# Kernel tuning notes

Measured on AMD Instinct MI355X. Metric: run time of the kernel, lower is better.

## Reference

```python
import jax, jax.numpy as jnp
import numpy as np

DEPTH = 4
EPS = 1e-05


def _hard_sigmoid(x):
    # Keras hard_sigmoid: clip(0.2*x + 0.5, 0, 1)
    return jnp.clip(0.2 * x + 0.5, 0.0, 1.0)


def _ln(x, gamma, beta):
    m = jnp.mean(x, axis=-1, keepdims=True)
    std = jnp.sqrt(jnp.var(x, axis=-1, keepdims=True) + EPS)
    return gamma * ((x - m) / (std + EPS)) + beta


def setup_inputs() -> dict:
    key = jax.random.key(0)
    ks = jax.random.split(key, 4)
    B, T, Din, H = 64, 256, 512, 512
    D = Din + H
    O = 2 * H + Din
    x = jax.random.normal(ks[0], (B, T, Din), dtype=jnp.float32)
    mask = jnp.ones((B, T), dtype=bool)
    W = jax.random.normal(ks[1], (D, O), dtype=jnp.float32) * (1.0 / np.sqrt(D))
    U = jax.random.normal(ks[2], (D, O), dtype=jnp.float32) * (1.0 / np.sqrt(D))
    b = jnp.zeros((O,), dtype=jnp.float32)
    gammas = jnp.ones((2, O), dtype=jnp.float32)
    betas = jnp.zeros((2, O), dtype=jnp.float32)
    return {"x": x, "mask": mask, "W": W, "U": U, "b": b,
            "gammas": gammas, "betas": betas, "bucket_size": 256}


def _forward(x, mask, W, U, b, gammas, betas, bucket_size):
    B, T, Din = x.shape
    D = W.shape[0]            # Din + H
    H = W.shape[1] - D        # hidden_dim
    # pad x with zeros in the hidden slots: (B,T,D) -> time-major (Tb,B,D)
    xp = jnp.concatenate([x, jnp.zeros((B, T, H), x.dtype)], axis=-1)
    xs = jnp.transpose(xp, (1, 0, 2))[:bucket_size]           # (Tb,B,D)
    m = jnp.transpose(mask, (1, 0))[:bucket_size]             # (Tb,B) bool
    # mask2 = mask * (1 - shift_left(mask)) : marks the last valid position
    m_shift = jnp.concatenate([m[1:], jnp.zeros((1, B), bool)], axis=0)
    m2 = jnp.logical_and(m, jnp.logical_not(m_shift))          # (Tb,B)
    mf = m.astype(x.dtype)[:, :, None]                         # (Tb,B,1)
    m2f = m2[:, :, None]                                       # (Tb,B,1) bool

    g0, g1 = gammas[0], gammas[1]
    be0, be1 = betas[0], betas[1]

    def hstep(carry, inp):
        h_tm1, fk_tm1 = carry
        xt, fkp, mt, m2t = inp
        sum1 = _ln(xt @ W, g0, be0)
        sum2 = _ln(h_tm1 @ U, g1, be1)
        total = sum1 + sum2 + b
        fk_c = _hard_sigmoid(total[:, :D])                     # (B,D)
        h_ = jnp.tanh(total[:, D:])                            # (B,H)
        h_pad = jnp.concatenate([jnp.zeros((xt.shape[0], D - H), xt.dtype), h_], axis=-1)
        h_cand = (1.0 - fk_c) * xt + fk_c * h_pad
        h = fkp * h_tm1 + (1.0 - fkp) * h_cand
        fk = fkp + (1.0 - fkp) * fk_c
        fk = jnp.where(m2t, 0.0, fk)
        out_h = mt * h + (1.0 - mt) * h_tm1
        out_fk = mt * fk + (1.0 - mt) * fk_tm1
        return (out_h, out_fk), (out_h, out_fk)

    Tb = xs.shape[0]
    fk_prev = jnp.zeros((Tb, B, D), x.dtype)
    h_seq = xs
    for _ in range(DEPTH):
        init = (jnp.zeros((B, D), x.dtype), jnp.zeros((B, D), x.dtype))
        _, (h_seq, fk_seq) = jax.lax.scan(hstep, init, (h_seq, fk_prev, mf, m2f))
        fk_prev = jnp.concatenate([fk_seq[1:], jnp.zeros((1, B, D), x.dtype)], axis=0)
    # outputs = last depth, last timestep, hidden slice
    return h_seq[-1, :, Din:]                                  # (B,H)


def reference(x, mask, W, U, b, gammas, betas, bucket_size):
    return _forward(x, mask, W, U, b, gammas, betas, bucket_size)
```

## Files before the change

### kernel.cpp

```cpp
#include <hip/hip_runtime.h>
#include <hip/hip_bf16.h>
#include <math.h>

#define B_   64
#define T_   256
#define DIN_ 512
#define H_   512
#define D_   1024
#define O_   1536
#define TB_  (T_*B_)
#define EPSf 1e-5f
#define NWG  96
#define NSLOT (T_ + 6)

typedef short  bf16x8 __attribute__((ext_vector_type(8)));
typedef float  f32x4  __attribute__((ext_vector_type(4)));
typedef ushort u16x4  __attribute__((ext_vector_type(4)));
typedef unsigned long long ull;

#define SPLIT1(f, Hm, Lm) { __hip_bfloat16 _h = __float2bfloat16(f); (Hm) = *(ushort*)&_h; \
    __hip_bfloat16 _l = __float2bfloat16((f) - __bfloat162float(_h)); (Lm) = *(ushort*)&_l; }

__device__ inline void st_f32_coh(float* p, float v) {
    __hip_atomic_store(p, v, __ATOMIC_RELAXED, __HIP_MEMORY_SCOPE_AGENT);
}
__device__ inline void st_u16_coh(ushort* p, ushort v) {
    __hip_atomic_store(p, v, __ATOMIC_RELAXED, __HIP_MEMORY_SCOPE_AGENT);
}
__device__ inline void st_u32_coh(unsigned* p, unsigned v) {
    __hip_atomic_store(p, v, __ATOMIC_RELAXED, __HIP_MEMORY_SCOPE_AGENT);
}
__device__ inline void st_f32x2_coh(float* p, float a, float b) {
    union { float f[2]; ull u; } pk;
    pk.f[0] = a; pk.f[1] = b;
    __hip_atomic_store((ull*)p, pk.u, __ATOMIC_RELAXED, __HIP_MEMORY_SCOPE_AGENT);
}

__global__ __launch_bounds__(256) void k_mask(const int* __restrict__ mask,
                                              int* __restrict__ mcode) {
    int g = blockIdx.x * 256 + threadIdx.x;
    int t = g >> 6, b = g & 63;
    int mt = mask[b * T_ + t] != 0;
    int mn = (t + 1 < T_) ? (mask[b * T_ + t + 1] != 0) : 0;
    mcode[g] = mt | (mn << 1);
}

__global__ __launch_bounds__(256) void k_prepx(const float* __restrict__ x,
                                               ushort* __restrict__ Xh) {
    int g  = blockIdx.x * 256 + threadIdx.x;
    int i4 = g * 4;
    int row = i4 >> 10;
    int k   = i4 & 1023;
    int t = row >> 6, b = row & 63;
    float4 v = make_float4(0.f, 0.f, 0.f, 0.f);
    if (k < 512) v = *(const float4*)&x[((size_t)b * T_ + t) * 512 + k];
    u16x4 h;
    __hip_bfloat16 b0 = __float2bfloat16(v.x); h[0] = *(ushort*)&b0;
    __hip_bfloat16 b1 = __float2bfloat16(v.y); h[1] = *(ushort*)&b1;
    __hip_bfloat16 b2 = __float2bfloat16(v.z); h[2] = *(ushort*)&b2;
    __hip_bfloat16 b3 = __float2bfloat16(v.w); h[3] = *(ushort*)&b3;
    *(u16x4*)&Xh[i4] = h;
}

__global__ __launch_bounds__(256) void k_prep(const float* __restrict__ M,
                                              ushort* __restrict__ Mt_hi,
                                              ushort* __restrict__ Mt_lo) {
    __shared__ float ls[64][65];
    int k0 = blockIdx.y * 64;
    int o0 = blockIdx.x * 64;
    int tid = threadIdx.x;
    int r = tid >> 2, cq = tid & 3;
#pragma unroll
    for (int j = 0; j < 4; ++j) {
        float4 v = *(const float4*)&M[(size_t)(k0 + r) * O_ + o0 + cq * 16 + j * 4];
        ls[r][cq * 16 + j * 4 + 0] = v.x;
        ls[r][cq * 16 + j * 4 + 1] = v.y;
        ls[r][cq * 16 + j * 4 + 2] = v.z;
        ls[r][cq * 16 + j * 4 + 3] = v.w;
    }
    __syncthreads();
    int ol = tid >> 2, kq = tid & 3;
    ushort th[16], tl[16];
#pragma unroll
    for (int j = 0; j < 16; ++j) {
        float v = ls[kq * 16 + j][ol];
        SPLIT1(v, th[j], tl[j]);
    }
    size_t base = (size_t)(o0 + ol) * D_ + k0 + kq * 16;
    *(int4*)&Mt_hi[base]     = *(int4*)&th[0];
    *(int4*)&Mt_hi[base + 8] = *(int4*)&th[8];
    *(int4*)&Mt_lo[base]     = *(int4*)&tl[0];
    *(int4*)&Mt_lo[base + 8] = *(int4*)&tl[8];
}

__device__ inline void gbar(unsigned* __restrict__ fl, int w, unsigned bar) {
    __syncthreads();
    asm volatile("s_waitcnt vmcnt(0)" ::: "memory");
    if (threadIdx.x == 0)
        __hip_atomic_store(&fl[w], bar, __ATOMIC_RELAXED, __HIP_MEMORY_SCOPE_AGENT);
    if (threadIdx.x < NWG) {
        while (__hip_atomic_load(&fl[threadIdx.x], __ATOMIC_RELAXED,
                                 __HIP_MEMORY_SCOPE_AGENT) < bar)
            __builtin_amdgcn_s_sleep(2);
    }
    __syncthreads();
    __builtin_amdgcn_fence(__ATOMIC_ACQUIRE, "agent");
}

__global__ __launch_bounds__(256, 1) void k_pipe(
        const float* __restrict__ x,
        const ushort* __restrict__ Xbh,
        ushort* __restrict__ Xrh,
        ushort* __restrict__ Hbh,
        float* __restrict__ Y1, float* __restrict__ Y2,
        float* __restrict__ pstats, float* __restrict__ finals,
        unsigned* __restrict__ ftag, unsigned* __restrict__ flags,
        const ushort* __restrict__ Uth, const ushort* __restrict__ Utl,
        const ushort* __restrict__ Wth, const ushort* __restrict__ Wtl,
        const float* __restrict__ gam, const float* __restrict__ bet,
        const float* __restrict__ bias,
        const int* __restrict__ mcode, float* __restrict__ out) {
    __shared__ __hip_bfloat16 lds[4 * 16 * 1024];
    __shared__ f32x4 ldsc[2][64][2];
    const int bx = blockIdx.x;
    const int dom = bx / NWG;
    const int w   = bx % NWG;
    const int tid = threadIdx.x;
    const int lane = tid & 63;
    const int wv = tid >> 6;
    const int rt = wv & 1;
    const int kh = wv >> 1;
    const int lr = lane & 15;
    const int lg = lane >> 4;
    const int c0 = w * 16;
    const int br0 = dom * 32 + rt * 16;
    unsigned* fl = flags + dom * 128;
    float* pst   = pstats + (size_t)dom * 4 * 32 * NWG * 4;
    float* fin   = finals + (size_t)dom * 128 * 4;
    unsigned* ft = ftag + (size_t)dom * 128;

    {
        int cl = tid >> 4, kc = tid & 15;
        const ushort* srcs0 = Uth + (size_t)(c0 + cl) * D_ + kc * 64;
        const ushort* srcs1 = Utl + (size_t)(c0 + cl) * D_ + kc * 64;
        const ushort* srcs2 = Wth + (size_t)(c0 + cl) * D_ + kc * 64;
        const ushort* srcs3 = Wtl + (size_t)(c0 + cl) * D_ + kc * 64;
        char* base = (char*)lds;
#pragma unroll
        for (int j = 0; j < 8; ++j) {
            int k = kc * 64 + j * 8;
            int off = (cl * 2048 + k * 2) ^ ((cl & 7) << 4);
            *(int4*)(base + off)           = *(const int4*)(srcs0 + j * 8);
            *(int4*)(base + 32768 + off)   = *(const int4*)(srcs1 + j * 8);
            *(int4*)(base + 65536 + off)   = *(const int4*)(srcs2 + j * 8);
            *(int4*)(base + 98304 + off)   = *(const int4*)(srcs3 + j * 8);
        }
    }
    __syncthreads();

    const int d = c0 + lr;
    const bool gate_w = (w < 64);
    const bool tanh_w = (w >= 32 && w < 64);
    float g0d = 0.f, g1d = 0.f, cd = 0.f, g0e = 0.f, g1e = 0.f, ce = 0.f;
    if (gate_w) {
        g0d = gam[d]; g1d = gam[O_ + d];
        cd  = bet[d] + bet[O_ + d] + bias[d];
    }
    if (tanh_w) {
        int e = d + 512;
        g0e = gam[e]; g1e = gam[O_ + e];
        ce  = bet[e] + bet[O_ + e] + bias[e];
    }

    float h1r[4][4] = {}, fk1r[4][4] = {};
    float oh_d1[4][4] = {}, oh_d2[4][4] = {}, fkp_d1[4][4] = {};
    f32x4 acc1[4], acc2[4];

    unsigned bar = 0;
    for (int s = 0; s < NSLOT; ++s) {
#pragma unroll
        for (int l = 0; l < 4; ++l) {
            int t = s - 2 * l;
            bool act = (t >= 0) && (t < T_);
            f32x4 p1 = {0,0,0,0}, p2 = {0,0,0,0};
            if (act) {
                const ushort* xsh;
                if (l == 0) {
                    xsh = Xbh + ((size_t)t * B_ + br0 + lr) * D_ + kh * 512;
                } else {
                    xsh = Xrh + (((size_t)l * 3 + (t % 3)) * B_ + br0 + lr) * D_ + kh * 512;
                }
                const ushort* hsh = Hbh + ((size_t)l * B_ + br0 + lr) * D_ + kh * 512;
                const char* lb = (const char*)lds;
                f32x4 a10 = {0,0,0,0}, a11 = {0,0,0,0};
                f32x4 a20 = {0,0,0,0}, a21 = {0,0,0,0};
#pragma unroll 4
                for (int kc = 0; kc < 16; ++kc) {
                    int kloc = kc * 32 + lg * 8;
                    int kglob = kh * 512 + kloc;
                    int off = (lr * 2048 + kglob * 2) ^ ((lr & 7) << 4);
                    bf16x8 xa = *(const bf16x8*)(xsh + kloc);
                    bf16x8 ha = *(const bf16x8*)(hsh + kloc);
                    bf16x8 ubh = *(const bf16x8*)(lb + off);
                    bf16x8 ubl = *(const bf16x8*)(lb + 32768 + off);
                    bf16x8 wbh = *(const bf16x8*)(lb + 65536 + off);
                    bf16x8 wbl = *(const bf16x8*)(lb + 98304 + off);
                    a10 = __builtin_amdgcn_mfma_f32_16x16x32_bf16(xa, wbh, a10, 0, 0, 0);
                    a11 = __builtin_amdgcn_mfma_f32_16x16x32_bf16(xa, wbl, a11, 0, 0, 0);
                    a20 = __builtin_amdgcn_mfma_f32_16x16x32_bf16(ha, ubh, a20, 0, 0, 0);
                    a21 = __builtin_amdgcn_mfma_f32_16x16x32_bf16(ha, ubl, a21, 0, 0, 0);
                }
                p1 = a10 + a11;
                p2 = a20 + a21;
                if (kh == 1) { ldsc[rt][lane][0] = p1; ldsc[rt][lane][1] = p2; }
            }
            __syncthreads();
            if (act && kh == 0) {
                f32x4 o1 = ldsc[rt][lane][0], o2 = ldsc[rt][lane][1];
                acc1[l] = p1 + o1;
                acc2[l] = p2 + o2;
#pragma unroll
                for (int j = 0; j < 4; ++j) {
                    float s1 = acc1[l][j], q1 = s1 * s1;
                    float s2 = acc2[l][j], q2 = s2 * s2;
#pragma unroll
                    for (int m = 1; m < 16; m <<= 1) {
                        s1 += __shfl_xor(s1, m); q1 += __shfl_xor(q1, m);
                        s2 += __shfl_xor(s2, m); q2 += __shfl_xor(q2, m);
                    }
                    if (lr == 0) {
                        int lrow = rt * 16 + lg * 4 + j;
                        float* sp = &pst[(((size_t)l * 32 + lrow) * NWG + w) * 4];
                        st_f32x2_coh(sp, s1, q1);
                        st_f32x2_coh(sp + 2, s2, q2);
                    }
                }
                if (w >= 64) {
                    int cexp = c0 + lr - 1024;
#pragma unroll
                    for (int j = 0; j < 4; ++j) {
                        int b = br0 + lg * 4 + j;
                        st_f32_coh(&Y1[((size_t)l * B_ + b) * 512 + cexp], acc1[l][j]);
                        st_f32_coh(&Y2[((size_t)l * B_ + b) * 512 + cexp], acc2[l][j]);
                    }
                }
            }
            __syncthreads();
        }
        gbar(fl, w, ++bar);

        if (wv < 2) {
            int pair = w + NWG * wv;
            if (pair < 128) {
                const float* pp = &pst[(size_t)pair * NWG * 4];
                float s1 = 0.f, q1 = 0.f, s2 = 0.f, q2 = 0.f;
                if (lane < 32) {
#pragma unroll
                    for (int i = 0; i < 3; ++i) {
                        float4 v = *(const float4*)(pp + (lane + i * 32) * 4);
                        s1 += v.x; q1 += v.y; s2 += v.z; q2 += v.w;
                    }
                }
#pragma unroll
                for (int m = 1; m < 32; m <<= 1) {
                    s1 += __shfl_xor(s1, m); q1 += __shfl_xor(q1, m);
                    s2 += __shfl_xor(s2, m); q2 += __shfl_xor(q2, m);
                }
                if (lane == 0) {
                    float m1 = s1 * (1.f / O_);
                    float v1 = q1 * (1.f / O_) - m1 * m1;
                    float i1 = 1.f / (sqrtf(v1 + EPSf) + EPSf);
                    float m2 = s2 * (1.f / O_);
                    float v2 = q2 * (1.f / O_) - m2 * m2;
                    float i2 = 1.f / (sqrtf(v2 + EPSf) + EPSf);
                    st_f32x2_coh(&fin[(size_t)pair * 4], m1, i1);
                    st_f32x2_coh(&fin[(size_t)pair * 4 + 2], m2, i2);
                    asm volatile("s_waitcnt vmcnt(0)" ::: "memory");
                    st_u32_coh(&ft[pair], (unsigned)(s + 1));
                }
            }
        }

        if (gate_w && wv < 2) {
#pragma unroll
            for (int li = 0; li < 4; ++li) {
                const int l = 3 - li;
                const int lp = (l > 0) ? l - 1 : 0;
                int t = s - 2 * l;
                bool act = (t >= 0) && (t < T_);
                float ohn[4], ofkn[4];
                if (act) {
                    int b_base = dom * 32 + wv * 16 + lg * 4;
                    int4 mc4 = *(const int4*)&mcode[t * B_ + b_base];
                    int mcarr[4] = {mc4.x, mc4.y, mc4.z, mc4.w};
#pragma unroll
                    for (int j = 0; j < 4; ++j) {
                        int b = b_base + j;
                        int lrow = wv * 16 + lg * 4 + j;
                        int pair = l * 32 + lrow;
                        while (__hip_atomic_load(&ft[pair], __ATOMIC_RELAXED,
                                                 __HIP_MEMORY_SCOPE_AGENT) < (unsigned)(s + 1))
                            __builtin_amdgcn_s_sleep(1);
                        union { ull u[2]; float f[4]; } fv;
                        fv.u[0] = __hip_atomic_load((ull*)&fin[(size_t)pair * 4],
                                                    __ATOMIC_RELAXED, __HIP_MEMORY_SCOPE_AGENT);
                        fv.u[1] = __hip_atomic_load((ull*)&fin[(size_t)pair * 4 + 2],
                                                    __ATOMIC_RELAXED, __HIP_MEMORY_SCOPE_AGENT);
                        float m1 = fv.f[0], i1 = fv.f[1], m2 = fv.f[2], i2 = fv.f[3];
                        float y1 = acc1[l][j], y2 = acc2[l][j];
                        float td = g0d * (y1 - m1) * i1 + g1d * (y2 - m2) * i2 + cd;
                        float fkc = fminf(fmaxf(0.2f * td + 0.5f, 0.f), 1.f);
                        float hpad = 0.f;
                        if (tanh_w) {
                            float y1e = Y1[((size_t)l * B_ + b) * 512 + (d - 512)];
                            float y2e = Y2[((size_t)l * B_ + b) * 512 + (d - 512)];
                            float te = g0e * (y1e - m1) * i1 + g1e * (y2e - m2) * i2 + ce;
                            hpad = tanhf(te);
                        }
                        float xt;
                        if (l == 0)
                            xt = (d < 512) ? x[((size_t)b * T_ + t) * 512 + d] : 0.f;
                        else
                            xt = oh_d2[lp][j];
                        float fkp = (l > 0 && t + 1 < T_) ? fkp_d1[lp][j] : 0.f;
                        float hc = (1.f - fkc) * xt + fkc * hpad;
                        float h  = fkp * h1r[l][j] + (1.f - fkp) * hc;
                        float fk = fkp + (1.f - fkp) * fkc;
                        int mt = mcarr[j] & 1, mn = (mcarr[j] >> 1) & 1;
                        if (mt && !mn) fk = 0.f;
                        float oh  = mt ? h  : h1r[l][j];
                        float ofk = mt ? fk : fk1r[l][j];
                        h1r[l][j] = oh; fk1r[l][j] = ofk;
                        __hip_bfloat16 hb = __float2bfloat16(oh);
                        ushort hi = *(ushort*)&hb;
                        st_u16_coh(Hbh + ((size_t)l * B_ + b) * D_ + d, hi);
                        if (l < 3) {
                            size_t xb = (((size_t)(l + 1) * 3 + (t % 3)) * B_ + b) * D_ + d;
                            st_u16_coh(Xrh + xb, hi);
                        }
                        if (l == 3 && t == T_ - 1 && d >= 512)
                            out[(size_t)b * 512 + (d - 512)] = oh;
                        ohn[j] = oh; ofkn[j] = ofk;
                    }
                }
#pragma unroll
                for (int j = 0; j < 4; ++j) {
                    oh_d2[l][j] = oh_d1[l][j];
                    if (act) { oh_d1[l][j] = ohn[j]; fkp_d1[l][j] = ofkn[j]; }
                }
            }
        }
        gbar(fl, w, ++bar);
    }
}

extern "C" void kernel_launch(void* const* d_in, const int* in_sizes, int n_in,
                              void* d_out, int out_size, void* d_ws, size_t ws_size,
                              hipStream_t stream) {
    (void)in_sizes; (void)n_in; (void)out_size;
    const float* x      = (const float*)d_in[0];
    const int*   mask   = (const int*)d_in[1];
    const float* W      = (const float*)d_in[2];
    const float* U      = (const float*)d_in[3];
    const float* bias   = (const float*)d_in[4];
    const float* gammas = (const float*)d_in[5];
    const float* betas  = (const float*)d_in[6];

    float* ws = (float*)d_ws;
    float* Y1    = ws;
    float* Y2    = Y1 + (size_t)4 * B_ * 512;
    float* pstats = Y2 + (size_t)4 * B_ * 512;
    float* finals = pstats + (size_t)2 * 4 * 32 * NWG * 4;
    unsigned* ftag  = (unsigned*)(finals + 2 * 128 * 4);
    unsigned* flags = ftag + 2 * 128;
    int* mcode = (int*)(flags + 256);
    ushort* Xbh = (ushort*)(mcode + TB_);
    ushort* Xrh = Xbh + (size_t)TB_ * D_;
    ushort* Hbh = Xrh + (size_t)4 * 3 * B_ * D_;
    ushort* Uth = Hbh + (size_t)4 * B_ * D_;
    ushort* Utl = Uth + (size_t)O_ * D_;
    ushort* Wth = Utl + (size_t)O_ * D_;
    ushort* Wtl = Wth + (size_t)O_ * D_;
    size_t need_bytes = ((char*)(Wtl + (size_t)O_ * D_)) - ((char*)d_ws);
    if (ws_size < need_bytes) return;

    k_prepx<<<TB_ * D_ / 4 / 256, 256, 0, stream>>>(x, Xbh);
    k_mask<<<TB_ / 256, 256, 0, stream>>>(mask, mcode);
    k_prep<<<dim3(O_ / 64, D_ / 64), 256, 0, stream>>>(U, Uth, Utl);
    k_prep<<<dim3(O_ / 64, D_ / 64), 256, 0, stream>>>(W, Wth, Wtl);
    (void)hipMemsetAsync(Hbh, 0, sizeof(ushort) * (size_t)4 * B_ * D_, stream);
    (void)hipMemsetAsync(pstats, 0, sizeof(float) * (size_t)2 * 4 * 32 * NWG * 4, stream);
    (void)hipMemsetAsync(ftag, 0, sizeof(unsigned) * 2 * 128, stream);
    (void)hipMemsetAsync(flags, 0, sizeof(unsigned) * 256, stream);

    k_pipe<<<2 * NWG, 256, 0, stream>>>(x, Xbh, Xrh, Hbh,
                                        Y1, Y2, pstats, finals, ftag, flags,
                                        Uth, Utl, Wth, Wtl,
                                        gammas, betas, bias, mcode, (float*)d_out);
}
```

Baseline: 15.32 ms.

## Batch per-depth partial reductions to one barrier and interleave domain block mapping

Gives each depth level its own LDS slot for the k-half partial sums, so all four levels' MFMA work runs before a single __syncthreads instead of two barriers per level. The LN statistics pass then runs over all levels after that one barrier, which lets the MFMA chains of different levels overlap and removes seven block barriers per time slot. Separately, the block-to-domain mapping changes from contiguous to interleaved (dom = bx&1), which changes how the two domains are spread across CUs. The cost is more registers for holding p1/p2 across four levels and extra LDS for the partial-sum staging.

```diff
diff --git a/kernel.cpp b/kernel.cpp
--- a/kernel.cpp
+++ b/kernel.cpp
@@ -121,10 +121,10 @@
         const float* __restrict__ bias,
         const int* __restrict__ mcode, float* __restrict__ out) {
     __shared__ __hip_bfloat16 lds[4 * 16 * 1024];
-    __shared__ f32x4 ldsc[2][64][2];
+    __shared__ f32x4 ldsc[4][2][64][2];
     const int bx = blockIdx.x;
-    const int dom = bx / NWG;
-    const int w   = bx % NWG;
+    const int dom = bx & 1;
+    const int w   = bx >> 1;
     const int tid = threadIdx.x;
     const int lane = tid & 63;
     const int wv = tid >> 6;
@@ -178,11 +178,13 @@
 
     unsigned bar = 0;
     for (int s = 0; s < NSLOT; ++s) {
+        f32x4 p1[4], p2[4];
 #pragma unroll
         for (int l = 0; l < 4; ++l) {
             int t = s - 2 * l;
             bool act = (t >= 0) && (t < T_);
-            f32x4 p1 = {0,0,0,0}, p2 = {0,0,0,0};
+            p1[l] = (f32x4){0,0,0,0};
+            p2[l] = (f32x4){0,0,0,0};
             if (act) {
                 const ushort* xsh;
                 if (l == 0) {
@@ -210,15 +212,23 @@
                     a20 = __builtin_amdgcn_mfma_f32_16x16x32_bf16(ha, ubh, a20, 0, 0, 0);
                     a21 = __builtin_amdgcn_mfma_f32_16x16x32_bf16(ha, ubl, a21, 0, 0, 0);
                 }
-                p1 = a10 + a11;
-                p2 = a20 + a21;
-                if (kh == 1) { ldsc[rt][lane][0] = p1; ldsc[rt][lane][1] = p2; }
+                p1[l] = a10 + a11;
+                p2[l] = a20 + a21;
+                if (kh == 1) {
+                    ldsc[l][rt][lane][0] = p1[l];
+                    ldsc[l][rt][lane][1] = p2[l];
+                }
             }
-            __syncthreads();
-            if (act && kh == 0) {
-                f32x4 o1 = ldsc[rt][lane][0], o2 = ldsc[rt][lane][1];
-                acc1[l] = p1 + o1;
-                acc2[l] = p2 + o2;
+        }
+        __syncthreads();
+        if (kh == 0) {
+#pragma unroll
+            for (int l = 0; l < 4; ++l) {
+                int t = s - 2 * l;
+                bool act = (t >= 0) && (t < T_);
+                if (!act) continue;
+                acc1[l] = p1[l] + ldsc[l][rt][lane][0];
+                acc2[l] = p2[l] + ldsc[l][rt][lane][1];
 #pragma unroll
                 for (int j = 0; j < 4; ++j) {
                     float s1 = acc1[l][j], q1 = s1 * s1;
@@ -245,7 +255,6 @@
                     }
                 }
             }
-            __syncthreads();
         }
         gbar(fl, w, ++bar);
 
```

New measurement: 15.15 ms. No clear change (-1.0%).
